# Kernel optimization log

Hardware: AMD Instinct MI355X
Metric: run time of the kernel (lower is better)

Reference implementation:

```python
import jax, jax.numpy as jnp
import numpy as np

HID = 64
PRE = 14


def _lstm_last(x, Wih, Whh, b):
    # x: (B, T, F) batch_first; single-layer torch LSTM; returns last hidden (B, H)
    H = Whh.shape[1]
    def step(carry, xt):
        h, c = carry
        g = xt @ Wih.T + h @ Whh.T + b  # gates order i,f,g,o (torch convention)
        i, f, gg, o = jnp.split(g, 4, axis=-1)
        c = jax.nn.sigmoid(f) * c + jax.nn.sigmoid(i) * jnp.tanh(gg)
        h = jax.nn.sigmoid(o) * jnp.tanh(c)
        return (h, c), None
    h0 = jnp.zeros((x.shape[0], H), x.dtype)
    (h, _), _ = jax.lax.scan(step, (h0, h0), jnp.swapaxes(x, 0, 1))
    return h


def _sircell(beta, gamma, c, sir):
    # beta,gamma: (B,N,1); c: (B,N,N); sir: (B,N,3); beta_incorporated=False branch
    eps = 1e-8
    S, I, R = sir[..., 0:1], sir[..., 1:2], sir[..., 2:3]
    Ntot = jnp.maximum(S + I + R, eps)
    infection = c @ I                      # (B,N,1) graph diffusion of infected
    dS = -beta * S / Ntot * infection
    dI = -dS - gamma * I
    dR = gamma * I
    S_t = jnp.maximum(S + dS, 0.0)
    I_t = jnp.maximum(I + dI, 0.0)
    R_t = jnp.maximum(R + dR, 0.0)
    scale = Ntot / jnp.maximum(S_t + I_t + R_t, eps)
    I_new = jnp.maximum(-dS, 0.0)
    return jnp.concatenate([I_new, S_t * scale, I_t * scale, R_t * scale], axis=-1)


def reference(x_s, x, bWih, bWhh, bb, bfW, bfb, gWih, gWhh, gb, gfW, gfb, cWih, cWhh, cb, cfW, cfb):
    B, T, N, F = x_s.shape
    P = bfW.shape[0]
    xs = jnp.transpose(x_s, (0, 2, 1, 3)).reshape(B * N, T, F)
    betas = jax.nn.sigmoid(_lstm_last(xs, bWih, bWhh, bb) @ bfW.T + bfb).reshape(B, N, P, 1)
    gammas = jax.nn.sigmoid(_lstm_last(xs, gWih, gWhh, gb) @ gfW.T + gfb).reshape(B, N, P, 1)
    xst = jnp.transpose(x_s, (0, 2, 1, 3))                       # (B,N,T,F)
    Hi = jnp.broadcast_to(xst[:, :, None], (B, N, N, T, F))
    Hj = jnp.broadcast_to(xst[:, None], (B, N, N, T, F))
    edge = jnp.concatenate([Hi, Hj], -1).reshape(B * N * N, T, 2 * F)
    cij = jax.nn.sigmoid(_lstm_last(edge, cWih, cWhh, cb) @ cfW.T + cfb).reshape(B, N, N, P)
    cij = jax.nn.softmax(jnp.transpose(cij, (0, 3, 1, 2)), axis=-1)  # (B,P,N,N)
    cs = jnp.transpose(cij, (0, 2, 1, 3))                            # (B,N,P,N)

    def step(sir, inp):
        bt, gt, ct = inp
        nsir = _sircell(bt, gt, ct, sir)
        return nsir[:, :, 1:], nsir

    _, outs = jax.lax.scan(
        step, x[:, -1],
        (jnp.transpose(betas, (2, 0, 1, 3)),
         jnp.transpose(gammas, (2, 0, 1, 3)),
         jnp.transpose(cs, (2, 0, 1, 3))))
    out = jnp.transpose(outs, (1, 0, 2, 3))                          # (B,P,N,4)
    epi = jnp.transpose(jnp.concatenate([betas, gammas, cs], -1), (0, 2, 1, 3))  # (B,P,N,N+2)
    return out[..., 2:3], epi, out[..., 1:], out[..., 0:1]


def setup_inputs() -> dict:
    key = jax.random.key(0)
    ks = jax.random.split(key, 20)
    B, T, N, F = 4, 12, 128, 3
    H, P = HID, PRE
    s = 1.0 / np.sqrt(H)
    def u(k, shape):
        return jax.random.uniform(k, shape, jnp.float32, -s, s)
    inp = {
        'x_s': jax.random.normal(ks[0], (B, T, N, F), jnp.float32),
        'x': jax.random.uniform(ks[1], (B, T, N, F), jnp.float32),
        'bWih': u(ks[2], (4 * H, F)), 'bWhh': u(ks[3], (4 * H, H)), 'bb': u(ks[4], (4 * H,)),
        'bfW': u(ks[5], (P, H)), 'bfb': u(ks[6], (P,)),
        'gWih': u(ks[7], (4 * H, F)), 'gWhh': u(ks[8], (4 * H, H)), 'gb': u(ks[9], (4 * H,)),
        'gfW': u(ks[10], (P, H)), 'gfb': u(ks[11], (P,)),
        'cWih': u(ks[12], (4 * H, 2 * F)), 'cWhh': u(ks[13], (4 * H, H)), 'cb': u(ks[14], (4 * H,)),
        'cfW': u(ks[15], (P, H)), 'cfb': u(ks[16], (P,)),
    }
    return inp
```

## Files before the change

### kernel.cpp

```cpp
#include <hip/hip_runtime.h>

#define TT 12
#define NN 128
#define BB 4
#define PP 14

typedef __attribute__((ext_vector_type(8))) short short8;
typedef __attribute__((ext_vector_type(4))) float f32x4;
typedef __attribute__((ext_vector_type(2))) float float2v;
typedef __attribute__((ext_vector_type(2))) unsigned uint2v;

__device__ inline unsigned short f2bf(float x){
  unsigned u = __builtin_bit_cast(unsigned, x);
  u += 0x7fffu + ((u >> 16) & 1u);
  return (unsigned short)(u >> 16);
}
__device__ inline float bf2f(unsigned short h){
  unsigned u = ((unsigned)h) << 16;
  return __builtin_bit_cast(float, u);
}
__device__ inline float fexp2(float x){ return __builtin_amdgcn_exp2f(x); }
__device__ inline float sigf(float x){ return __builtin_amdgcn_rcpf(1.0f + fexp2(x * -1.44269504f)); }

__device__ inline float2v exp2v(float2v x){
  float2v r; r[0]=__builtin_amdgcn_exp2f(x[0]); r[1]=__builtin_amdgcn_exp2f(x[1]); return r;
}
__device__ inline float2v rcpv(float2v x){
  float2v r; r[0]=__builtin_amdgcn_rcpf(x[0]); r[1]=__builtin_amdgcn_rcpf(x[1]); return r;
}
__device__ inline float2v sigp(float2v xp){ return rcpv(1.0f + exp2v(xp)); }
__device__ inline float2v tanhp(float2v xp){ return 1.0f - 2.0f*rcpv(1.0f + exp2v(xp)); }

__global__ __launch_bounds__(256) void lstm_all(
    const float* __restrict__ x_s,
    const float* __restrict__ bWih, const float* __restrict__ bWhh, const float* __restrict__ bb_,
    const float* __restrict__ bfW,  const float* __restrict__ bfb,
    const float* __restrict__ gWih, const float* __restrict__ gWhh, const float* __restrict__ gb_,
    const float* __restrict__ gfW,  const float* __restrict__ gfb,
    const float* __restrict__ cWih, const float* __restrict__ cWhh, const float* __restrict__ cb_,
    const float* __restrict__ cfW,  const float* __restrict__ cfb,
    float* __restrict__ out_epi,
    float* __restrict__ betas_ws, float* __restrict__ gammas_ws)
{
  __shared__ __align__(16) char hbuf[2*2048];
  __shared__ __align__(16) unsigned short xext[TT*16*8];
  __shared__ float fw_lds[PP*64];
  __shared__ float fb_lds[PP];

  const int tid = threadIdx.x;
  const int l = tid & 63, w = tid >> 6;
  const int col = l & 15, q = l >> 4;

  const int rot = (col & 7) << 4;
  const int r0off = col*128 + ((  0 + (q<<4) + rot) & 127);
  const int r1off = col*128 + (( 64 + (q<<4) + rot) & 127);
  const int wroff = col*128 + ((w*32 + q*8 + rot) & 127);

  short8 Aw[4][2]; short8 Ax[4];
  int pmode = -1;
  const short8 zero8 = {0,0,0,0,0,0,0,0};

  for (int it = 0; it < 2; ++it) {
    int g = blockIdx.x + it*2080;

    int mode; const float *Wih, *Whh, *bias, *fW, *fb;
    if (g < 4096)      { mode=0; Wih=cWih; Whh=cWhh; bias=cb_; fW=cfW; fb=cfb; }
    else if (g < 4128) { mode=1; g-=4096; Wih=bWih; Whh=bWhh; bias=bb_; fW=bfW; fb=bfb; }
    else               { mode=2; g-=4128; Wih=gWih; Whh=gWhh; bias=gb_; fW=gfW; fb=gfb; }

    int b, i=0, j0=0, n0=0;
    if (mode==0) { b = g >> 10; int rem = g & 1023; i = rem >> 3; j0 = (rem & 7) << 4; }
    else         { b = g >> 3; n0 = (g & 7) << 4; }

    __syncthreads();

    if (mode != pmode) {
      pmode = mode;
      for (int idx = tid; idx < PP*64; idx += 256) fw_lds[idx] = fW[idx];
      if (tid < PP) fb_lds[tid] = fb[tid];
      #pragma unroll
      for (int gt = 0; gt < 4; ++gt) {
        float sc = (gt==2) ? 2.88539008f : -1.44269504f;
        int gate = gt*64 + w*16 + col;
        #pragma unroll
        for (int kt = 0; kt < 2; ++kt) {
          const float* src = Whh + gate*64 + kt*32 + q*8;
          short8 fr;
          #pragma unroll
          for (int jj = 0; jj < 8; ++jj) fr[jj] = (short)f2bf(src[jj]*sc);
          Aw[gt][kt] = fr;
        }
        short8 ax = {0,0,0,0,0,0,0,0};
        if (q == 0) {
          if (mode==0) {
            ax[0]=(short)f2bf(Wih[gate*6+0]*sc); ax[1]=(short)f2bf(Wih[gate*6+1]*sc); ax[2]=(short)f2bf(Wih[gate*6+2]*sc);
            ax[3]=(short)f2bf(Wih[gate*6+3]*sc); ax[4]=(short)f2bf(Wih[gate*6+4]*sc); ax[5]=(short)f2bf(Wih[gate*6+5]*sc);
            ax[6]=(short)f2bf(bias[gate]*sc);
          } else {
            ax[0]=(short)f2bf(Wih[gate*3+0]*sc); ax[1]=(short)f2bf(Wih[gate*3+1]*sc); ax[2]=(short)f2bf(Wih[gate*3+2]*sc);
            ax[3]=(short)f2bf(bias[gate]*sc);
          }
        }
        Ax[gt] = ax;
      }
    }

    for (int task = tid; task < TT*16; task += 256) {
      int t = task >> 4, m = task & 15;
      unsigned short* dst = &xext[(t*16+m)*8];
      float v0=0,v1=0,v2=0,v3=0,v4=0,v5=0,v6=0,v7=0;
      if (mode==0) {
        const float* xi = x_s + ((b*TT + t)*NN + i)*3;
        const float* xj = x_s + ((b*TT + t)*NN + (j0+m))*3;
        v0=xi[0]; v1=xi[1]; v2=xi[2]; v3=xj[0]; v4=xj[1]; v5=xj[2]; v6=1.f;
      } else {
        const float* xn = x_s + ((b*TT + t)*NN + (n0+m))*3;
        v0=xn[0]; v1=xn[1]; v2=xn[2]; v3=1.f;
      }
      dst[0]=f2bf(v0); dst[1]=f2bf(v1); dst[2]=f2bf(v2); dst[3]=f2bf(v3);
      dst[4]=f2bf(v4); dst[5]=f2bf(v5); dst[6]=f2bf(v6); dst[7]=f2bf(v7);
    }
    for (int idx = tid; idx < 512; idx += 256) ((unsigned*)hbuf)[idx] = 0;

    __syncthreads();

    float2v c0 = {0.f,0.f}, c1 = {0.f,0.f};

    for (int t = 0; t < TT; ++t) {
      const char* rb = hbuf + ((t & 1) ? 2048 : 0);
      char* wbp      = hbuf + ((t & 1) ? 0 : 2048);
      short8 b0 = *(const short8*)(rb + r0off);
      short8 b1 = *(const short8*)(rb + r1off);
      short8 bx = zero8;
      if (l < 16) bx = *(const short8*)&xext[(t*16 + col)*8];
      f32x4 Fi = {0.f,0.f,0.f,0.f}, Ii = Fi, Gi = Fi, Oi = Fi;
      Fi = __builtin_amdgcn_mfma_f32_16x16x32_bf16(Aw[1][0], b0, Fi, 0,0,0);
      Fi = __builtin_amdgcn_mfma_f32_16x16x32_bf16(Aw[1][1], b1, Fi, 0,0,0);
      Fi = __builtin_amdgcn_mfma_f32_16x16x32_bf16(Ax[1],    bx, Fi, 0,0,0);
      Ii = __builtin_amdgcn_mfma_f32_16x16x32_bf16(Aw[0][0], b0, Ii, 0,0,0);
      Ii = __builtin_amdgcn_mfma_f32_16x16x32_bf16(Aw[0][1], b1, Ii, 0,0,0);
      Ii = __builtin_amdgcn_mfma_f32_16x16x32_bf16(Ax[0],    bx, Ii, 0,0,0);
      Gi = __builtin_amdgcn_mfma_f32_16x16x32_bf16(Aw[2][0], b0, Gi, 0,0,0);
      Gi = __builtin_amdgcn_mfma_f32_16x16x32_bf16(Aw[2][1], b1, Gi, 0,0,0);
      Gi = __builtin_amdgcn_mfma_f32_16x16x32_bf16(Ax[2],    bx, Gi, 0,0,0);
      Oi = __builtin_amdgcn_mfma_f32_16x16x32_bf16(Aw[3][0], b0, Oi, 0,0,0);
      Oi = __builtin_amdgcn_mfma_f32_16x16x32_bf16(Aw[3][1], b1, Oi, 0,0,0);
      Oi = __builtin_amdgcn_mfma_f32_16x16x32_bf16(Ax[3],    bx, Oi, 0,0,0);

      float2v f0 = {Fi[0],Fi[1]}, f1 = {Fi[2],Fi[3]};
      float2v i0 = {Ii[0],Ii[1]}, i1 = {Ii[2],Ii[3]};
      float2v g0 = {Gi[0],Gi[1]}, g1 = {Gi[2],Gi[3]};
      float2v o0 = {Oi[0],Oi[1]}, o1 = {Oi[2],Oi[3]};
      c0 = sigp(f0)*c0 + sigp(i0)*tanhp(g0);
      c1 = sigp(f1)*c1 + sigp(i1)*tanhp(g1);
      float2v tc0 = 1.0f - 2.0f*rcpv(1.0f + exp2v(c0 * 2.88539008f));
      float2v tc1 = 1.0f - 2.0f*rcpv(1.0f + exp2v(c1 * 2.88539008f));
      float2v h0 = sigp(o0)*tc0;
      float2v h1 = sigp(o1)*tc1;
      unsigned plo, phi;
      asm("v_cvt_pk_bf16_f32 %0, %1, %2" : "=v"(plo) : "v"(h0[0]), "v"(h0[1]));
      asm("v_cvt_pk_bf16_f32 %0, %1, %2" : "=v"(phi) : "v"(h1[0]), "v"(h1[1]));
      uint2v pv = {plo, phi};
      *(uint2v*)(wbp + wroff) = pv;
      __syncthreads();
    }

    const char* hfin = hbuf;
    for (int task = tid; task < 16*PP; task += 256) {
      int seq = task & 15, p = task >> 4;
      int rot2 = (seq & 7) << 4;
      float dot = fb_lds[p];
      #pragma unroll
      for (int kc = 0; kc < 8; ++kc) {
        short8 v = *(const short8*)(hfin + seq*128 + (((kc<<4) + rot2) & 127));
        #pragma unroll
        for (int jj = 0; jj < 8; ++jj)
          dot += bf2f((unsigned short)v[jj]) * fw_lds[p*64 + kc*8 + jj];
      }
      float val = sigf(dot);
      if (mode==0) {
        out_epi[(size_t)((b*PP + p)*NN + i)*130 + 2 + (j0+seq)] = val;
      } else if (mode==1) {
        betas_ws[(b*NN + n0+seq)*PP + p] = val;
      } else {
        gammas_ws[(b*NN + n0+seq)*PP + p] = val;
      }
    }
  }
}

__global__ __launch_bounds__(256) void softmax_epi(
    const float* __restrict__ betas_ws, const float* __restrict__ gammas_ws,
    float* __restrict__ out_epi)
{
  int row = blockIdx.x*4 + (threadIdx.x >> 6);
  int l = threadIdx.x & 63;
  int b = row / (PP*NN); int rem = row - b*(PP*NN); int p = rem >> 7; int i = rem & 127;
  float* epi = out_epi + (size_t)row*130;
  float v0 = epi[2+l], v1 = epi[2+64+l];
  float m = fmaxf(v0, v1);
  #pragma unroll
  for (int off = 32; off; off >>= 1) m = fmaxf(m, __shfl_xor(m, off));
  float e0 = fexp2((v0-m)*1.44269504f), e1 = fexp2((v1-m)*1.44269504f);
  float s = e0 + e1;
  #pragma unroll
  for (int off = 32; off; off >>= 1) s += __shfl_xor(s, off);
  float inv = 1.0f / s;
  epi[2+l] = e0*inv; epi[2+64+l] = e1*inv;
  if (l == 0) epi[0] = betas_ws[(b*NN+i)*PP + p];
  if (l == 1) epi[1] = gammas_ws[(b*NN+i)*PP + p];
}

__global__ __launch_bounds__(1024) void sir_scan(
    const float* __restrict__ x,
    const float* __restrict__ betas_ws, const float* __restrict__ gammas_ws,
    const float* __restrict__ epi,
    float* __restrict__ out0, float* __restrict__ out2, float* __restrict__ out3)
{
  __shared__ float Ish[NN];
  int b = blockIdx.x;
  int tid = threadIdx.x;
  int i = tid >> 3, q = tid & 7;
  const float* x0 = x + ((b*TT + 11)*NN + i)*3;
  float S = x0[0], I = x0[1], R = x0[2];
  if (q == 0) Ish[i] = I;

  float2v v[8], vn[8];
  {
    const float* crow = epi + (size_t)((b*PP + 0)*NN + i)*130 + 2 + q*16;
    #pragma unroll
    for (int jj = 0; jj < 8; ++jj) v[jj] = *(const float2v*)(crow + jj*2);
  }
  __syncthreads();
  for (int p = 0; p < PP; ++p) {
    if (p+1 < PP) {
      const float* crow = epi + (size_t)((b*PP + p+1)*NN + i)*130 + 2 + q*16;
      #pragma unroll
      for (int jj = 0; jj < 8; ++jj) vn[jj] = *(const float2v*)(crow + jj*2);
    }
    float part = 0.f;
    #pragma unroll
    for (int jj = 0; jj < 8; ++jj)
      part += v[jj][0]*Ish[q*16 + jj*2] + v[jj][1]*Ish[q*16 + jj*2 + 1];
    part += __shfl_xor(part, 1);
    part += __shfl_xor(part, 2);
    part += __shfl_xor(part, 4);
    __syncthreads();
    if (q == 0) {
      float beta  = betas_ws[(b*NN+i)*PP + p];
      float gamma = gammas_ws[(b*NN+i)*PP + p];
      float Ntot = fmaxf(S+I+R, 1e-8f);
      float dS = -beta*S/Ntot*part;
      float dI = -dS - gamma*I;
      float dR = gamma*I;
      float St = fmaxf(S+dS, 0.f), It = fmaxf(I+dI, 0.f), Rt = fmaxf(R+dR, 0.f);
      float scale = Ntot / fmaxf(St+It+Rt, 1e-8f);
      float Inew = fmaxf(-dS, 0.f);
      int o = (b*PP+p)*NN + i;
      float Sn = St*scale, In = It*scale, Rn = Rt*scale;
      out0[o] = In;
      out2[o*3+0] = Sn; out2[o*3+1] = In; out2[o*3+2] = Rn;
      out3[o] = Inew;
      S = Sn; I = In; R = Rn;
      Ish[i] = I;
    }
    #pragma unroll
    for (int jj = 0; jj < 8; ++jj) v[jj] = vn[jj];
    __syncthreads();
  }
}

extern "C" void kernel_launch(void* const* d_in, const int* in_sizes, int n_in,
                              void* d_out, int out_size, void* d_ws, size_t ws_size,
                              hipStream_t stream) {
  const float* x_s  = (const float*)d_in[0];
  const float* x    = (const float*)d_in[1];
  const float* bWih = (const float*)d_in[2];
  const float* bWhh = (const float*)d_in[3];
  const float* bb_  = (const float*)d_in[4];
  const float* bfW  = (const float*)d_in[5];
  const float* bfb  = (const float*)d_in[6];
  const float* gWih = (const float*)d_in[7];
  const float* gWhh = (const float*)d_in[8];
  const float* gb_  = (const float*)d_in[9];
  const float* gfW  = (const float*)d_in[10];
  const float* gfb  = (const float*)d_in[11];
  const float* cWih = (const float*)d_in[12];
  const float* cWhh = (const float*)d_in[13];
  const float* cb_  = (const float*)d_in[14];
  const float* cfW  = (const float*)d_in[15];
  const float* cfb  = (const float*)d_in[16];

  float* out  = (float*)d_out;
  float* out0 = out;
  float* epi  = out + 7168;
  float* out2 = out + 7168 + 931840;
  float* out3 = out + 7168 + 931840 + 21504;
  float* betas_ws  = (float*)d_ws;
  float* gammas_ws = betas_ws + 7168;

  hipLaunchKernelGGL(lstm_all, dim3(2080), dim3(256), 0, stream,
      x_s, bWih,bWhh,bb_,bfW,bfb, gWih,gWhh,gb_,gfW,gfb, cWih,cWhh,cb_,cfW,cfb,
      epi, betas_ws, gammas_ws);
  hipLaunchKernelGGL(softmax_epi, dim3(1792), dim3(256), 0, stream,
      betas_ws, gammas_ws, epi);
  hipLaunchKernelGGL(sir_scan, dim3(4), dim3(1024), 0, stream,
      x, betas_ws, gammas_ws, epi, out0, out2, out3);
}
```

Measured before the change: 120.0 us.

## Process two 16-sequence groups per block with interleaved MFMA chains

Each block now handles two adjacent 16-sequence tiles at once instead of looping over two tiles one after the other. The MFMA chains for the two tiles are interleaved so their instructions hide each other's latency, and the per-step barrier is shared between both. This halves the number of serial timestep loops and barriers per block and drops the weight reload across iterations. In exchange it doubles LDS for the hidden and input buffers and raises register pressure, which may lower occupancy. The host launch grid presumably has to change to match the new block-to-work mapping.

```diff
diff --git a/kernel.cpp b/kernel.cpp
--- a/kernel.cpp
+++ b/kernel.cpp
@@ -42,8 +42,8 @@
     float* __restrict__ out_epi,
     float* __restrict__ betas_ws, float* __restrict__ gammas_ws)
 {
-  __shared__ __align__(16) char hbuf[2*2048];
-  __shared__ __align__(16) unsigned short xext[TT*16*8];
+  __shared__ __align__(16) char hbuf[2*4096];
+  __shared__ __align__(16) unsigned short xext[TT*32*8];
   __shared__ float fw_lds[PP*64];
   __shared__ float fb_lds[PP];
 
@@ -52,139 +52,160 @@
   const int col = l & 15, q = l >> 4;
 
   const int rot = (col & 7) << 4;
-  const int r0off = col*128 + ((  0 + (q<<4) + rot) & 127);
-  const int r1off = col*128 + (( 64 + (q<<4) + rot) & 127);
-  const int wroff = col*128 + ((w*32 + q*8 + rot) & 127);
+  const int r0offA = col*128 + ((  0 + (q<<4) + rot) & 127);
+  const int r1offA = col*128 + (( 64 + (q<<4) + rot) & 127);
+  const int wroffA = col*128 + ((w*32 + q*8 + rot) & 127);
+  const int r0offB = r0offA + 2048;
+  const int r1offB = r1offA + 2048;
+  const int wroffB = wroffA + 2048;
+
+  int g0 = blockIdx.x << 1;
+  int mode; const float *Wih, *Whh, *bias, *fW, *fb;
+  if (g0 < 4096)      { mode=0; Wih=cWih; Whh=cWhh; bias=cb_; fW=cfW; fb=cfb; }
+  else if (g0 < 4128) { mode=1; g0-=4096; Wih=bWih; Whh=bWhh; bias=bb_; fW=bfW; fb=bfb; }
+  else                { mode=2; g0-=4128; Wih=gWih; Whh=gWhh; bias=gb_; fW=gfW; fb=gfb; }
+
+  int b, i=0, s0;
+  if (mode==0) { b = g0 >> 10; int rem = g0 & 1023; i = rem >> 3; s0 = (rem & 7) << 4; }
+  else         { b = g0 >> 3; s0 = (g0 & 7) << 4; }
+
+  for (int task = tid; task < TT*32; task += 256) {
+    int t = task >> 5, m = task & 31;
+    unsigned short* dst = &xext[(t*32+m)*8];
+    float v0=0,v1=0,v2=0,v3=0,v4=0,v5=0,v6=0,v7=0;
+    if (mode==0) {
+      const float* xi = x_s + ((b*TT + t)*NN + i)*3;
+      const float* xj = x_s + ((b*TT + t)*NN + (s0+m))*3;
+      v0=xi[0]; v1=xi[1]; v2=xi[2]; v3=xj[0]; v4=xj[1]; v5=xj[2]; v6=1.f;
+    } else {
+      const float* xn = x_s + ((b*TT + t)*NN + (s0+m))*3;
+      v0=xn[0]; v1=xn[1]; v2=xn[2]; v3=1.f;
+    }
+    dst[0]=f2bf(v0); dst[1]=f2bf(v1); dst[2]=f2bf(v2); dst[3]=f2bf(v3);
+    dst[4]=f2bf(v4); dst[5]=f2bf(v5); dst[6]=f2bf(v6); dst[7]=f2bf(v7);
+  }
+  for (int idx = tid; idx < 1024; idx += 256) ((unsigned*)hbuf)[idx] = 0;
+  for (int idx = tid; idx < PP*64; idx += 256) fw_lds[idx] = fW[idx];
+  if (tid < PP) fb_lds[tid] = fb[tid];
 
   short8 Aw[4][2]; short8 Ax[4];
-  int pmode = -1;
+  #pragma unroll
+  for (int gt = 0; gt < 4; ++gt) {
+    float sc = (gt==2) ? 2.88539008f : -1.44269504f;
+    int gate = gt*64 + w*16 + col;
+    #pragma unroll
+    for (int kt = 0; kt < 2; ++kt) {
+      const float* src = Whh + gate*64 + kt*32 + q*8;
+      short8 fr;
+      #pragma unroll
+      for (int jj = 0; jj < 8; ++jj) fr[jj] = (short)f2bf(src[jj]*sc);
+      Aw[gt][kt] = fr;
+    }
+    short8 ax = {0,0,0,0,0,0,0,0};
+    if (q == 0) {
+      if (mode==0) {
+        ax[0]=(short)f2bf(Wih[gate*6+0]*sc); ax[1]=(short)f2bf(Wih[gate*6+1]*sc); ax[2]=(short)f2bf(Wih[gate*6+2]*sc);
+        ax[3]=(short)f2bf(Wih[gate*6+3]*sc); ax[4]=(short)f2bf(Wih[gate*6+4]*sc); ax[5]=(short)f2bf(Wih[gate*6+5]*sc);
+        ax[6]=(short)f2bf(bias[gate]*sc);
+      } else {
+        ax[0]=(short)f2bf(Wih[gate*3+0]*sc); ax[1]=(short)f2bf(Wih[gate*3+1]*sc); ax[2]=(short)f2bf(Wih[gate*3+2]*sc);
+        ax[3]=(short)f2bf(bias[gate]*sc);
+      }
+    }
+    Ax[gt] = ax;
+  }
+
+  __syncthreads();
+
+  float2v cA0 = {0.f,0.f}, cA1 = {0.f,0.f}, cB0 = {0.f,0.f}, cB1 = {0.f,0.f};
   const short8 zero8 = {0,0,0,0,0,0,0,0};
 
-  for (int it = 0; it < 2; ++it) {
-    int g = blockIdx.x + it*2080;
-
-    int mode; const float *Wih, *Whh, *bias, *fW, *fb;
-    if (g < 4096)      { mode=0; Wih=cWih; Whh=cWhh; bias=cb_; fW=cfW; fb=cfb; }
-    else if (g < 4128) { mode=1; g-=4096; Wih=bWih; Whh=bWhh; bias=bb_; fW=bfW; fb=bfb; }
-    else               { mode=2; g-=4128; Wih=gWih; Whh=gWhh; bias=gb_; fW=gfW; fb=gfb; }
-
-    int b, i=0, j0=0, n0=0;
-    if (mode==0) { b = g >> 10; int rem = g & 1023; i = rem >> 3; j0 = (rem & 7) << 4; }
-    else         { b = g >> 3; n0 = (g & 7) << 4; }
-
-    __syncthreads();
-
-    if (mode != pmode) {
-      pmode = mode;
-      for (int idx = tid; idx < PP*64; idx += 256) fw_lds[idx] = fW[idx];
-      if (tid < PP) fb_lds[tid] = fb[tid];
-      #pragma unroll
-      for (int gt = 0; gt < 4; ++gt) {
-        float sc = (gt==2) ? 2.88539008f : -1.44269504f;
-        int gate = gt*64 + w*16 + col;
-        #pragma unroll
-        for (int kt = 0; kt < 2; ++kt) {
-          const float* src = Whh + gate*64 + kt*32 + q*8;
-          short8 fr;
-          #pragma unroll
-          for (int jj = 0; jj < 8; ++jj) fr[jj] = (short)f2bf(src[jj]*sc);
-          Aw[gt][kt] = fr;
-        }
-        short8 ax = {0,0,0,0,0,0,0,0};
-        if (q == 0) {
-          if (mode==0) {
-            ax[0]=(short)f2bf(Wih[gate*6+0]*sc); ax[1]=(short)f2bf(Wih[gate*6+1]*sc); ax[2]=(short)f2bf(Wih[gate*6+2]*sc);
-            ax[3]=(short)f2bf(Wih[gate*6+3]*sc); ax[4]=(short)f2bf(Wih[gate*6+4]*sc); ax[5]=(short)f2bf(Wih[gate*6+5]*sc);
-            ax[6]=(short)f2bf(bias[gate]*sc);
-          } else {
-            ax[0]=(short)f2bf(Wih[gate*3+0]*sc); ax[1]=(short)f2bf(Wih[gate*3+1]*sc); ax[2]=(short)f2bf(Wih[gate*3+2]*sc);
-            ax[3]=(short)f2bf(bias[gate]*sc);
-          }
-        }
-        Ax[gt] = ax;
-      }
-    }
-
-    for (int task = tid; task < TT*16; task += 256) {
-      int t = task >> 4, m = task & 15;
-      unsigned short* dst = &xext[(t*16+m)*8];
-      float v0=0,v1=0,v2=0,v3=0,v4=0,v5=0,v6=0,v7=0;
-      if (mode==0) {
-        const float* xi = x_s + ((b*TT + t)*NN + i)*3;
-        const float* xj = x_s + ((b*TT + t)*NN + (j0+m))*3;
-        v0=xi[0]; v1=xi[1]; v2=xi[2]; v3=xj[0]; v4=xj[1]; v5=xj[2]; v6=1.f;
-      } else {
-        const float* xn = x_s + ((b*TT + t)*NN + (n0+m))*3;
-        v0=xn[0]; v1=xn[1]; v2=xn[2]; v3=1.f;
-      }
-      dst[0]=f2bf(v0); dst[1]=f2bf(v1); dst[2]=f2bf(v2); dst[3]=f2bf(v3);
-      dst[4]=f2bf(v4); dst[5]=f2bf(v5); dst[6]=f2bf(v6); dst[7]=f2bf(v7);
-    }
-    for (int idx = tid; idx < 512; idx += 256) ((unsigned*)hbuf)[idx] = 0;
-
-    __syncthreads();
-
-    float2v c0 = {0.f,0.f}, c1 = {0.f,0.f};
-
-    for (int t = 0; t < TT; ++t) {
-      const char* rb = hbuf + ((t & 1) ? 2048 : 0);
-      char* wbp      = hbuf + ((t & 1) ? 0 : 2048);
-      short8 b0 = *(const short8*)(rb + r0off);
-      short8 b1 = *(const short8*)(rb + r1off);
-      short8 bx = zero8;
-      if (l < 16) bx = *(const short8*)&xext[(t*16 + col)*8];
-      f32x4 Fi = {0.f,0.f,0.f,0.f}, Ii = Fi, Gi = Fi, Oi = Fi;
-      Fi = __builtin_amdgcn_mfma_f32_16x16x32_bf16(Aw[1][0], b0, Fi, 0,0,0);
-      Fi = __builtin_amdgcn_mfma_f32_16x16x32_bf16(Aw[1][1], b1, Fi, 0,0,0);
-      Fi = __builtin_amdgcn_mfma_f32_16x16x32_bf16(Ax[1],    bx, Fi, 0,0,0);
-      Ii = __builtin_amdgcn_mfma_f32_16x16x32_bf16(Aw[0][0], b0, Ii, 0,0,0);
-      Ii = __builtin_amdgcn_mfma_f32_16x16x32_bf16(Aw[0][1], b1, Ii, 0,0,0);
-      Ii = __builtin_amdgcn_mfma_f32_16x16x32_bf16(Ax[0],    bx, Ii, 0,0,0);
-      Gi = __builtin_amdgcn_mfma_f32_16x16x32_bf16(Aw[2][0], b0, Gi, 0,0,0);
-      Gi = __builtin_amdgcn_mfma_f32_16x16x32_bf16(Aw[2][1], b1, Gi, 0,0,0);
-      Gi = __builtin_amdgcn_mfma_f32_16x16x32_bf16(Ax[2],    bx, Gi, 0,0,0);
-      Oi = __builtin_amdgcn_mfma_f32_16x16x32_bf16(Aw[3][0], b0, Oi, 0,0,0);
-      Oi = __builtin_amdgcn_mfma_f32_16x16x32_bf16(Aw[3][1], b1, Oi, 0,0,0);
-      Oi = __builtin_amdgcn_mfma_f32_16x16x32_bf16(Ax[3],    bx, Oi, 0,0,0);
-
-      float2v f0 = {Fi[0],Fi[1]}, f1 = {Fi[2],Fi[3]};
-      float2v i0 = {Ii[0],Ii[1]}, i1 = {Ii[2],Ii[3]};
-      float2v g0 = {Gi[0],Gi[1]}, g1 = {Gi[2],Gi[3]};
-      float2v o0 = {Oi[0],Oi[1]}, o1 = {Oi[2],Oi[3]};
-      c0 = sigp(f0)*c0 + sigp(i0)*tanhp(g0);
-      c1 = sigp(f1)*c1 + sigp(i1)*tanhp(g1);
-      float2v tc0 = 1.0f - 2.0f*rcpv(1.0f + exp2v(c0 * 2.88539008f));
-      float2v tc1 = 1.0f - 2.0f*rcpv(1.0f + exp2v(c1 * 2.88539008f));
+#define MM(acc, aop, bop) acc = __builtin_amdgcn_mfma_f32_16x16x32_bf16(aop, bop, acc, 0,0,0)
+
+  for (int t = 0; t < TT; ++t) {
+    const char* rb = hbuf + ((t & 1) ? 4096 : 0);
+    char* wbp      = hbuf + ((t & 1) ? 0 : 4096);
+    short8 b0a = *(const short8*)(rb + r0offA);
+    short8 b1a = *(const short8*)(rb + r1offA);
+    short8 b0b = *(const short8*)(rb + r0offB);
+    short8 b1b = *(const short8*)(rb + r1offB);
+    short8 bxa = zero8, bxb = zero8;
+    if (l < 16) {
+      bxa = *(const short8*)&xext[(t*32 + col)*8];
+      bxb = *(const short8*)&xext[(t*32 + 16 + col)*8];
+    }
+    f32x4 Fa = {0.f,0.f,0.f,0.f}, Ia = Fa, Ga = Fa, Oa = Fa;
+    f32x4 Fb = Fa, Ib = Fa, Gb = Fa, Ob = Fa;
+    MM(Fa, Aw[1][0], b0a); MM(Fb, Aw[1][0], b0b);
+    MM(Ia, Aw[0][0], b0a); MM(Ib, Aw[0][0], b0b);
+    MM(Ga, Aw[2][0], b0a); MM(Gb, Aw[2][0], b0b);
+    MM(Oa, Aw[3][0], b0a); MM(Ob, Aw[3][0], b0b);
+    MM(Fa, Aw[1][1], b1a); MM(Fb, Aw[1][1], b1b);
+    MM(Ia, Aw[0][1], b1a); MM(Ib, Aw[0][1], b1b);
+    MM(Ga, Aw[2][1], b1a); MM(Gb, Aw[2][1], b1b);
+    MM(Oa, Aw[3][1], b1a); MM(Ob, Aw[3][1], b1b);
+    MM(Fa, Ax[1], bxa);    MM(Fb, Ax[1], bxb);
+    MM(Ia, Ax[0], bxa);    MM(Ib, Ax[0], bxb);
+    MM(Ga, Ax[2], bxa);    MM(Gb, Ax[2], bxb);
+    MM(Oa, Ax[3], bxa);    MM(Ob, Ax[3], bxb);
+
+    {
+      float2v f0 = {Fa[0],Fa[1]}, f1 = {Fa[2],Fa[3]};
+      float2v i0 = {Ia[0],Ia[1]}, i1 = {Ia[2],Ia[3]};
+      float2v g0v = {Ga[0],Ga[1]}, g1v = {Ga[2],Ga[3]};
+      float2v o0 = {Oa[0],Oa[1]}, o1 = {Oa[2],Oa[3]};
+      cA0 = sigp(f0)*cA0 + sigp(i0)*tanhp(g0v);
+      cA1 = sigp(f1)*cA1 + sigp(i1)*tanhp(g1v);
+      float2v tc0 = 1.0f - 2.0f*rcpv(1.0f + exp2v(cA0 * 2.88539008f));
+      float2v tc1 = 1.0f - 2.0f*rcpv(1.0f + exp2v(cA1 * 2.88539008f));
       float2v h0 = sigp(o0)*tc0;
       float2v h1 = sigp(o1)*tc1;
       unsigned plo, phi;
       asm("v_cvt_pk_bf16_f32 %0, %1, %2" : "=v"(plo) : "v"(h0[0]), "v"(h0[1]));
       asm("v_cvt_pk_bf16_f32 %0, %1, %2" : "=v"(phi) : "v"(h1[0]), "v"(h1[1]));
       uint2v pv = {plo, phi};
-      *(uint2v*)(wbp + wroff) = pv;
-      __syncthreads();
-    }
-
-    const char* hfin = hbuf;
-    for (int task = tid; task < 16*PP; task += 256) {
-      int seq = task & 15, p = task >> 4;
-      int rot2 = (seq & 7) << 4;
-      float dot = fb_lds[p];
+      *(uint2v*)(wbp + wroffA) = pv;
+    }
+    {
+      float2v f0 = {Fb[0],Fb[1]}, f1 = {Fb[2],Fb[3]};
+      float2v i0 = {Ib[0],Ib[1]}, i1 = {Ib[2],Ib[3]};
+      float2v g0v = {Gb[0],Gb[1]}, g1v = {Gb[2],Gb[3]};
+      float2v o0 = {Ob[0],Ob[1]}, o1 = {Ob[2],Ob[3]};
+      cB0 = sigp(f0)*cB0 + sigp(i0)*tanhp(g0v);
+      cB1 = sigp(f1)*cB1 + sigp(i1)*tanhp(g1v);
+      float2v tc0 = 1.0f - 2.0f*rcpv(1.0f + exp2v(cB0 * 2.88539008f));
+      float2v tc1 = 1.0f - 2.0f*rcpv(1.0f + exp2v(cB1 * 2.88539008f));
+      float2v h0 = sigp(o0)*tc0;
+      float2v h1 = sigp(o1)*tc1;
+      unsigned plo, phi;
+      asm("v_cvt_pk_bf16_f32 %0, %1, %2" : "=v"(plo) : "v"(h0[0]), "v"(h0[1]));
+      asm("v_cvt_pk_bf16_f32 %0, %1, %2" : "=v"(phi) : "v"(h1[0]), "v"(h1[1]));
+      uint2v pv = {plo, phi};
+      *(uint2v*)(wbp + wroffB) = pv;
+    }
+    __syncthreads();
+  }
+#undef MM
+
+  const char* hfin = hbuf;
+  for (int task = tid; task < 32*PP; task += 256) {
+    int seq = task & 31, p = task >> 5;
+    int rot2 = (seq & 7) << 4;
+    float dot = fb_lds[p];
+    #pragma unroll
+    for (int kc = 0; kc < 8; ++kc) {
+      short8 v = *(const short8*)(hfin + seq*128 + (((kc<<4) + rot2) & 127));
       #pragma unroll
-      for (int kc = 0; kc < 8; ++kc) {
-        short8 v = *(const short8*)(hfin + seq*128 + (((kc<<4) + rot2) & 127));
-        #pragma unroll
-        for (int jj = 0; jj < 8; ++jj)
-          dot += bf2f((unsigned short)v[jj]) * fw_lds[p*64 + kc*8 + jj];
-      }
-      float val = sigf(dot);
-      if (mode==0) {
-        out_epi[(size_t)((b*PP + p)*NN + i)*130 + 2 + (j0+seq)] = val;
-      } else if (mode==1) {
-        betas_ws[(b*NN + n0+seq)*PP + p] = val;
-      } else {
-        gammas_ws[(b*NN + n0+seq)*PP + p] = val;
-      }
+      for (int jj = 0; jj < 8; ++jj)
+        dot += bf2f((unsigned short)v[jj]) * fw_lds[p*64 + kc*8 + jj];
+    }
+    float val = sigf(dot);
+    if (mode==0) {
+      out_epi[(size_t)((b*PP + p)*NN + i)*130 + 2 + (s0+seq)] = val;
+    } else if (mode==1) {
+      betas_ws[(b*NN + s0+seq)*PP + p] = val;
+    } else {
+      gammas_ws[(b*NN + s0+seq)*PP + p] = val;
     }
   }
 }
```

After: 113.3 us. -5.6%, faster.
